# Kernel tuning notes

Measured on AMD Instinct MI355X. Metric: run time of the kernel, lower is better.

## Reference

```python
import jax, jax.numpy as jnp
import numpy as np


def setup_inputs() -> dict:
    key = jax.random.key(0)
    inputs = jax.random.normal(key, (4096, 8192), dtype=jnp.float32)
    return {"inputs": inputs, "k": 512}


def reference(inputs, k):
    # Original: kth_smallest = sort_ascending(inputs)[..., n-1-k]
    # i.e. the (k+1)-th largest value per row. Equivalent via top_k.
    # Keep only elements STRICTLY greater than that threshold.
    thresh = jax.lax.top_k(inputs, k + 1)[0][..., -1]  # [batch]
    mask = (inputs > thresh[:, None]).astype(inputs.dtype)
    return inputs * mask
```

## Files before the change

kernel.cpp:

```cpp
#include <hip/hip_runtime.h>
#include <stdint.h>


constexpr int COLS  = 8192;
constexpr int TPB   = 256;
constexpr int EPT   = COLS / TPB;
constexpr int VPT   = EPT / 4;
constexpr int NBIN0 = 2048;
constexpr int CAP   = 2048;

typedef float f32x4 __attribute__((ext_vector_type(4)));

__device__ __forceinline__ uint32_t map_f32(uint32_t u) {
  return (u & 0x80000000u) ? ~u : (u | 0x80000000u);
}
__device__ __forceinline__ float unmap_f32(uint32_t m) {
  return __uint_as_float((m & 0x80000000u) ? (m ^ 0x80000000u) : ~m);
}

template <int RPB>
__global__ __launch_bounds__(TPB, 4)
void ksparse_kernel(const float* __restrict__ in, const int* __restrict__ kptr,
                    float* __restrict__ out) {
  __shared__ __align__(16) uint32_t hist[2 * NBIN0];
  __shared__ uint32_t th[3 * 128];
  __shared__ uint32_t wtot[4];
  __shared__ uint32_t s_packed;
  __shared__ uint32_t s_cnt;
  __shared__ uint32_t s_sel[3];

  const int t    = threadIdx.x;
  const int wave = t >> 6;
  const int lane = t & 63;
  const size_t row0 = (size_t)blockIdx.x * RPB;

  const uint32_t kbase = (uint32_t)(*kptr) + 1u;

  float4   v[2][VPT];
  uint32_t m[EPT];

  {
    const float4* inp = (const float4*)(in + row0 * COLS);
#pragma unroll
    for (int i = 0; i < VPT; ++i) v[0][i] = inp[t + i * TPB];
  }

#pragma unroll
  for (int r = 0; r < RPB; ++r) {
    uint4* h4 = (uint4*)hist;
#pragma unroll
    for (int i = 0; i < 4; ++i) h4[t + i * TPB] = make_uint4(0u, 0u, 0u, 0u);
    th[t] = 0u;
    if (t < 128) th[256 + t] = 0u;
    if (t == 0) { s_packed = 0u; s_cnt = 0u; }
    uint32_t kk = kbase;
    __syncthreads();

    uint32_t* h = &hist[(wave >> 1) * NBIN0];
#pragma unroll
    for (int i = 0; i < VPT; ++i) {
      m[4 * i + 0] = map_f32(__float_as_uint(v[r & 1][i].x));
      m[4 * i + 1] = map_f32(__float_as_uint(v[r & 1][i].y));
      m[4 * i + 2] = map_f32(__float_as_uint(v[r & 1][i].z));
      m[4 * i + 3] = map_f32(__float_as_uint(v[r & 1][i].w));
      atomicAdd(&h[m[4 * i + 0] >> 21], 1u);
      atomicAdd(&h[m[4 * i + 1] >> 21], 1u);
      atomicAdd(&h[m[4 * i + 2] >> 21], 1u);
      atomicAdd(&h[m[4 * i + 3] >> 21], 1u);
    }

    if (r + 1 < RPB) {
      const float4* inp = (const float4*)(in + (row0 + (size_t)(r + 1)) * COLS);
#pragma unroll
      for (int i = 0; i < VPT; ++i) v[(r + 1) & 1][i] = inp[t + i * TPB];
    }
    __syncthreads();

    {
      const uint4* hv = (const uint4*)hist;
      uint4 a0 = hv[2 * t], a1 = hv[2 * t + 1];
      uint4 b0 = hv[512 + 2 * t], b1 = hv[512 + 2 * t + 1];
      uint32_t c0 = a0.x + b0.x, c1 = a0.y + b0.y, c2 = a0.z + b0.z, c3 = a0.w + b0.w;
      uint32_t c4 = a1.x + b1.x, c5 = a1.y + b1.y, c6 = a1.z + b1.z, c7 = a1.w + b1.w;
      uint32_t sl[8];
      sl[7] = c7;         sl[6] = sl[7] + c6; sl[5] = sl[6] + c5; sl[4] = sl[5] + c4;
      sl[3] = sl[4] + c3; sl[2] = sl[3] + c2; sl[1] = sl[2] + c1; sl[0] = sl[1] + c0;
      const uint32_t total = sl[0];

      uint32_t s = total;
#pragma unroll
      for (int off = 1; off < 64; off <<= 1) {
        uint32_t tmp = __shfl_down(s, off, 64);
        s += (lane + off < 64) ? tmp : 0u;
      }
      if (lane == 0) wtot[wave] = s;
      __syncthreads();

      uint32_t hi = 0;
#pragma unroll
      for (int w = 1; w < 4; ++w)
        if (w > wave) hi += wtot[w];
      const uint32_t excl = hi + (s - total);

      int best = -1;
#pragma unroll
      for (int j = 7; j >= 0; --j)
        if (best < 0 && excl + sl[j] >= kk) best = j;
      if (best >= 0) {
        const uint32_t above = excl + ((best < 7) ? sl[best + 1] : 0u);
        atomicMax(&s_packed, ((uint32_t)(t * 8 + best) << 14) | above);
      }
    }
    __syncthreads();

    const uint32_t pk = s_packed;
    const uint32_t d0 = pk >> 14;
    kk -= (pk & 0x3FFFu);

    uint32_t* cand = &hist[NBIN0];
#pragma unroll
    for (int i = 0; i < EPT; ++i) {
      if ((m[i] >> 21) == d0) {
        uint32_t idx = atomicAdd(&s_cnt, 1u);
        if (idx < CAP) cand[idx] = m[i] & 0x1FFFFFu;
      }
    }
    __syncthreads();
    const uint32_t Cc = (s_cnt < (uint32_t)CAP) ? s_cnt : (uint32_t)CAP;

    uint32_t tpref = 0;
#pragma unroll 1
    for (int j = 0; j < 3; ++j) {
      const int dsh = 14 - 7 * j;
      uint32_t* thj = &th[j * 128];
      for (uint32_t idx = t; idx < Cc; idx += TPB) {
        const uint32_t c = cand[idx];
        const bool ok = (j == 0) || ((c >> (dsh + 7)) == tpref);
        if (ok) atomicAdd(&thj[(c >> dsh) & 127u], 1u);
      }
      __syncthreads();

      if (wave == 0) {
        uint32_t a = thj[lane], b = thj[64 + lane];
        uint32_t sb = b, sa = a;
#pragma unroll
        for (int off = 1; off < 64; off <<= 1) {
          uint32_t t1 = __shfl_down(sb, off, 64);
          uint32_t t2 = __shfl_down(sa, off, 64);
          const bool inr = (lane + off < 64);
          sb += inr ? t1 : 0u;
          sa += inr ? t2 : 0u;
        }
        const uint32_t tb = __shfl(sb, 0, 64);
        sa += tb;
        const unsigned long long mb = __ballot(sb >= kk);
        uint32_t d, ab;
        if (mb) {
          const int hb = 63 - __builtin_clzll(mb);
          const uint32_t nx = __shfl(sb, (hb + 1) & 63, 64);
          d = 64 + hb;
          ab = (hb == 63) ? 0u : nx;
        } else {
          const unsigned long long ma = __ballot(sa >= kk);
          const int ha = 63 - __builtin_clzll(ma);
          const uint32_t nx = __shfl(sa, (ha + 1) & 63, 64);
          d = (uint32_t)ha;
          ab = (ha == 63) ? tb : nx;
        }
        if (lane == 0) s_sel[j] = (d << 16) | ab;
      }
      __syncthreads();

      const uint32_t sel = s_sel[j];
      tpref = (tpref << 7) | (sel >> 16);
      kk -= (sel & 0xFFFFu);
    }

    const uint32_t T = (d0 << 21) | tpref;

    f32x4* op = (f32x4*)(out + (row0 + (size_t)r) * COLS);
#pragma unroll
    for (int i = 0; i < VPT; ++i) {
      f32x4 w;
      uint32_t mm;
      mm = m[4 * i + 0]; w.x = (mm > T) ? unmap_f32(mm) : 0.0f;
      mm = m[4 * i + 1]; w.y = (mm > T) ? unmap_f32(mm) : 0.0f;
      mm = m[4 * i + 2]; w.z = (mm > T) ? unmap_f32(mm) : 0.0f;
      mm = m[4 * i + 3]; w.w = (mm > T) ? unmap_f32(mm) : 0.0f;
      __builtin_nontemporal_store(w, &op[t + i * TPB]);
    }
  }
}

extern "C" void kernel_launch(void* const* d_in, const int* in_sizes, int n_in,
                              void* d_out, int out_size, void* d_ws, size_t ws_size,
                              hipStream_t stream) {
  const float* in  = (const float*)d_in[0];
  const int*   k   = (const int*)d_in[1];
  float*       out = (float*)d_out;
  int rows = in_sizes[0] / COLS;
  if (rows < 1) rows = 1;
  if ((rows & 3) == 0) {
    ksparse_kernel<4><<<rows / 4, TPB, 0, stream>>>(in, k, out);
  } else {
    ksparse_kernel<1><<<rows, TPB, 0, stream>>>(in, k, out);
  }
}
```

Baseline: 258.7 us.

## Process rows of a block concurrently in lockstep instead of sequentially

Each block now handles two rows at once. Both rows are loaded up front and each gets its own histogram, and every selection phase runs for both rows between shared barriers, which halves the number of barrier-separated phases per row. The refinement scans run on separate waves per row. The per-wave split histogram is dropped, so histogram atomics contend on a single copy per row. Nontemporal output stores become plain stores. This holds more registers per thread (two rows of values and mapped keys) and doubles the block count, which can hurt occupancy.

```diff
diff --git a/kernel.cpp b/kernel.cpp
--- a/kernel.cpp
+++ b/kernel.cpp
@@ -9,8 +9,6 @@
 constexpr int NBIN0 = 2048;
 constexpr int CAP   = 2048;
 
-typedef float f32x4 __attribute__((ext_vector_type(4)));
-
 __device__ __forceinline__ uint32_t map_f32(uint32_t u) {
   return (u & 0x80000000u) ? ~u : (u | 0x80000000u);
 }
@@ -22,172 +20,204 @@
 __global__ __launch_bounds__(TPB, 4)
 void ksparse_kernel(const float* __restrict__ in, const int* __restrict__ kptr,
                     float* __restrict__ out) {
-  __shared__ __align__(16) uint32_t hist[2 * NBIN0];
-  __shared__ uint32_t th[3 * 128];
-  __shared__ uint32_t wtot[4];
-  __shared__ uint32_t s_packed;
-  __shared__ uint32_t s_cnt;
-  __shared__ uint32_t s_sel[3];
+  constexpr int NH = (RPB > 1) ? RPB : 2;
+  __shared__ __align__(16) uint32_t hist[NH * NBIN0];
+  __shared__ uint32_t th[RPB * 3 * 128];
+  __shared__ uint32_t wtot[RPB][4];
+  __shared__ uint32_t s_packed[RPB];
+  __shared__ uint32_t s_cnt[RPB];
+  __shared__ uint32_t s_sel[RPB][3];
 
   const int t    = threadIdx.x;
   const int wave = t >> 6;
   const int lane = t & 63;
-  const size_t row0 = (size_t)blockIdx.x * RPB;
-
+  const size_t rowbase = (size_t)blockIdx.x * RPB * COLS;
+
+  const float4* inp = (const float4*)(in + rowbase);
+  float4 v[RPB][VPT];
+#pragma unroll
+  for (int r = 0; r < RPB; ++r)
+#pragma unroll
+    for (int i = 0; i < VPT; ++i)
+      v[r][i] = inp[r * (COLS / 4) + t + i * TPB];
+
+  uint4* h4 = (uint4*)hist;
+#pragma unroll
+  for (int i = 0; i < NH * NBIN0 / 4 / TPB; ++i)
+    h4[t + i * TPB] = make_uint4(0u, 0u, 0u, 0u);
+#pragma unroll
+  for (int i = 0; i < (RPB * 384 + TPB - 1) / TPB; ++i) {
+    const int idx = t + i * TPB;
+    if (idx < RPB * 384) th[idx] = 0u;
+  }
+  if (t < RPB) { s_packed[t] = 0u; s_cnt[t] = 0u; }
   const uint32_t kbase = (uint32_t)(*kptr) + 1u;
-
-  float4   v[2][VPT];
-  uint32_t m[EPT];
-
-  {
-    const float4* inp = (const float4*)(in + row0 * COLS);
-#pragma unroll
-    for (int i = 0; i < VPT; ++i) v[0][i] = inp[t + i * TPB];
-  }
-
-#pragma unroll
-  for (int r = 0; r < RPB; ++r) {
-    uint4* h4 = (uint4*)hist;
-#pragma unroll
-    for (int i = 0; i < 4; ++i) h4[t + i * TPB] = make_uint4(0u, 0u, 0u, 0u);
-    th[t] = 0u;
-    if (t < 128) th[256 + t] = 0u;
-    if (t == 0) { s_packed = 0u; s_cnt = 0u; }
-    uint32_t kk = kbase;
+  __syncthreads();
+
+  uint32_t m[RPB][EPT];
+#pragma unroll
+  for (int r = 0; r < RPB; ++r) {
+    uint32_t* h = &hist[r * NBIN0];
+#pragma unroll
+    for (int i = 0; i < VPT; ++i) {
+      m[r][4 * i + 0] = map_f32(__float_as_uint(v[r][i].x));
+      m[r][4 * i + 1] = map_f32(__float_as_uint(v[r][i].y));
+      m[r][4 * i + 2] = map_f32(__float_as_uint(v[r][i].z));
+      m[r][4 * i + 3] = map_f32(__float_as_uint(v[r][i].w));
+      atomicAdd(&h[m[r][4 * i + 0] >> 21], 1u);
+      atomicAdd(&h[m[r][4 * i + 1] >> 21], 1u);
+      atomicAdd(&h[m[r][4 * i + 2] >> 21], 1u);
+      atomicAdd(&h[m[r][4 * i + 3] >> 21], 1u);
+    }
+  }
+  __syncthreads();
+
+  uint32_t kk[RPB];
+  uint32_t sl0[RPB];
+  uint32_t ssum[RPB];
+  uint4    sva0[RPB], sva1[RPB];
+#pragma unroll
+  for (int r = 0; r < RPB; ++r) {
+    kk[r] = kbase;
+    const uint4* hv = (const uint4*)&hist[r * NBIN0];
+    const uint4 a0 = hv[2 * t], a1 = hv[2 * t + 1];
+    sva0[r] = a0; sva1[r] = a1;
+    const uint32_t total = a0.x + a0.y + a0.z + a0.w + a1.x + a1.y + a1.z + a1.w;
+    sl0[r] = total;
+
+    uint32_t s = total;
+#pragma unroll
+    for (int off = 1; off < 64; off <<= 1) {
+      const uint32_t tmp = __shfl_down(s, off, 64);
+      s += (lane + off < 64) ? tmp : 0u;
+    }
+    ssum[r] = s;
+    if (lane == 0) wtot[r][wave] = s;
+  }
+  __syncthreads();
+
+#pragma unroll
+  for (int r = 0; r < RPB; ++r) {
+    uint32_t hi = 0;
+#pragma unroll
+    for (int w = 1; w < 4; ++w)
+      if (w > wave) hi += wtot[r][w];
+    const uint32_t excl = hi + (ssum[r] - sl0[r]);
+
+    const uint4 a0 = sva0[r], a1 = sva1[r];
+    uint32_t sl[8];
+    sl[7] = a1.w;         sl[6] = sl[7] + a1.z; sl[5] = sl[6] + a1.y; sl[4] = sl[5] + a1.x;
+    sl[3] = sl[4] + a0.w; sl[2] = sl[3] + a0.z; sl[1] = sl[2] + a0.y; sl[0] = sl[1] + a0.x;
+
+    int b = -1;
+#pragma unroll
+    for (int j = 7; j >= 0; --j)
+      if (b < 0 && excl + sl[j] >= kk[r]) b = j;
+    if (b >= 0) {
+      const uint32_t above = excl + ((b < 7) ? sl[b + 1] : 0u);
+      atomicMax(&s_packed[r], ((uint32_t)(t * 8 + b) << 14) | above);
+    }
+  }
+  __syncthreads();
+
+  uint32_t d0[RPB];
+#pragma unroll
+  for (int r = 0; r < RPB; ++r) {
+    const uint32_t pk = s_packed[r];
+    d0[r] = pk >> 14;
+    kk[r] -= (pk & 0x3FFFu);
+    uint32_t* cand = &hist[(RPB == 1 ? 1 : r) * NBIN0];
+#pragma unroll
+    for (int i = 0; i < EPT; ++i) {
+      if ((m[r][i] >> 21) == d0[r]) {
+        const uint32_t idx = atomicAdd(&s_cnt[r], 1u);
+        if (idx < CAP) cand[idx] = m[r][i] & 0x1FFFFFu;
+      }
+    }
+  }
+  __syncthreads();
+  uint32_t Cc[RPB];
+#pragma unroll
+  for (int r = 0; r < RPB; ++r)
+    Cc[r] = (s_cnt[r] < (uint32_t)CAP) ? s_cnt[r] : (uint32_t)CAP;
+
+  uint32_t tpref[RPB];
+#pragma unroll
+  for (int r = 0; r < RPB; ++r) tpref[r] = 0;
+
+#pragma unroll 1
+  for (int j = 0; j < 3; ++j) {
+    const int dsh = 14 - 7 * j;
+#pragma unroll
+    for (int r = 0; r < RPB; ++r) {
+      uint32_t* thj = &th[(r * 3 + j) * 128];
+      uint32_t* cand = &hist[(RPB == 1 ? 1 : r) * NBIN0];
+      for (uint32_t idx = t; idx < Cc[r]; idx += TPB) {
+        const uint32_t c = cand[idx];
+        const bool ok = (j == 0) || ((c >> (dsh + 7)) == tpref[r]);
+        if (ok) atomicAdd(&thj[(c >> dsh) & 127u], 1u);
+      }
+    }
     __syncthreads();
 
-    uint32_t* h = &hist[(wave >> 1) * NBIN0];
+    if (wave < RPB) {
+      uint32_t kw = 0;
+      uint32_t* thj = &th[j * 128];
+#pragma unroll
+      for (int r = 0; r < RPB; ++r)
+        if (wave == r) { kw = kk[r]; thj = &th[(r * 3 + j) * 128]; }
+
+      const uint32_t a = thj[lane], b = thj[64 + lane];
+      uint32_t sb = b, sa = a;
+#pragma unroll
+      for (int off = 1; off < 64; off <<= 1) {
+        const uint32_t t1 = __shfl_down(sb, off, 64);
+        const uint32_t t2 = __shfl_down(sa, off, 64);
+        const bool inr = (lane + off < 64);
+        sb += inr ? t1 : 0u;
+        sa += inr ? t2 : 0u;
+      }
+      const uint32_t tb = __shfl(sb, 0, 64);
+      sa += tb;
+      const unsigned long long mb = __ballot(sb >= kw);
+      uint32_t d, ab;
+      if (mb) {
+        const int hb = 63 - __builtin_clzll(mb);
+        const uint32_t nx = __shfl(sb, (hb + 1) & 63, 64);
+        d = 64 + (uint32_t)hb;
+        ab = (hb == 63) ? 0u : nx;
+      } else {
+        const unsigned long long ma = __ballot(sa >= kw);
+        const int ha = 63 - __builtin_clzll(ma);
+        const uint32_t nx = __shfl(sa, (ha + 1) & 63, 64);
+        d = (uint32_t)ha;
+        ab = (ha == 63) ? tb : nx;
+      }
+      if (lane == 0) s_sel[wave][j] = (d << 16) | ab;
+    }
+    __syncthreads();
+
+#pragma unroll
+    for (int r = 0; r < RPB; ++r) {
+      const uint32_t sel = s_sel[r][j];
+      tpref[r] = (tpref[r] << 7) | (sel >> 16);
+      kk[r] -= (sel & 0xFFFFu);
+    }
+  }
+
+  float4* op = (float4*)(out + rowbase);
+#pragma unroll
+  for (int r = 0; r < RPB; ++r) {
+    const uint32_t T = (d0[r] << 21) | tpref[r];
 #pragma unroll
     for (int i = 0; i < VPT; ++i) {
-      m[4 * i + 0] = map_f32(__float_as_uint(v[r & 1][i].x));
-      m[4 * i + 1] = map_f32(__float_as_uint(v[r & 1][i].y));
-      m[4 * i + 2] = map_f32(__float_as_uint(v[r & 1][i].z));
-      m[4 * i + 3] = map_f32(__float_as_uint(v[r & 1][i].w));
-      atomicAdd(&h[m[4 * i + 0] >> 21], 1u);
-      atomicAdd(&h[m[4 * i + 1] >> 21], 1u);
-      atomicAdd(&h[m[4 * i + 2] >> 21], 1u);
-      atomicAdd(&h[m[4 * i + 3] >> 21], 1u);
-    }
-
-    if (r + 1 < RPB) {
-      const float4* inp = (const float4*)(in + (row0 + (size_t)(r + 1)) * COLS);
-#pragma unroll
-      for (int i = 0; i < VPT; ++i) v[(r + 1) & 1][i] = inp[t + i * TPB];
-    }
-    __syncthreads();
-
-    {
-      const uint4* hv = (const uint4*)hist;
-      uint4 a0 = hv[2 * t], a1 = hv[2 * t + 1];
-      uint4 b0 = hv[512 + 2 * t], b1 = hv[512 + 2 * t + 1];
-      uint32_t c0 = a0.x + b0.x, c1 = a0.y + b0.y, c2 = a0.z + b0.z, c3 = a0.w + b0.w;
-      uint32_t c4 = a1.x + b1.x, c5 = a1.y + b1.y, c6 = a1.z + b1.z, c7 = a1.w + b1.w;
-      uint32_t sl[8];
-      sl[7] = c7;         sl[6] = sl[7] + c6; sl[5] = sl[6] + c5; sl[4] = sl[5] + c4;
-      sl[3] = sl[4] + c3; sl[2] = sl[3] + c2; sl[1] = sl[2] + c1; sl[0] = sl[1] + c0;
-      const uint32_t total = sl[0];
-
-      uint32_t s = total;
-#pragma unroll
-      for (int off = 1; off < 64; off <<= 1) {
-        uint32_t tmp = __shfl_down(s, off, 64);
-        s += (lane + off < 64) ? tmp : 0u;
-      }
-      if (lane == 0) wtot[wave] = s;
-      __syncthreads();
-
-      uint32_t hi = 0;
-#pragma unroll
-      for (int w = 1; w < 4; ++w)
-        if (w > wave) hi += wtot[w];
-      const uint32_t excl = hi + (s - total);
-
-      int best = -1;
-#pragma unroll
-      for (int j = 7; j >= 0; --j)
-        if (best < 0 && excl + sl[j] >= kk) best = j;
-      if (best >= 0) {
-        const uint32_t above = excl + ((best < 7) ? sl[best + 1] : 0u);
-        atomicMax(&s_packed, ((uint32_t)(t * 8 + best) << 14) | above);
-      }
-    }
-    __syncthreads();
-
-    const uint32_t pk = s_packed;
-    const uint32_t d0 = pk >> 14;
-    kk -= (pk & 0x3FFFu);
-
-    uint32_t* cand = &hist[NBIN0];
-#pragma unroll
-    for (int i = 0; i < EPT; ++i) {
-      if ((m[i] >> 21) == d0) {
-        uint32_t idx = atomicAdd(&s_cnt, 1u);
-        if (idx < CAP) cand[idx] = m[i] & 0x1FFFFFu;
-      }
-    }
-    __syncthreads();
-    const uint32_t Cc = (s_cnt < (uint32_t)CAP) ? s_cnt : (uint32_t)CAP;
-
-    uint32_t tpref = 0;
-#pragma unroll 1
-    for (int j = 0; j < 3; ++j) {
-      const int dsh = 14 - 7 * j;
-      uint32_t* thj = &th[j * 128];
-      for (uint32_t idx = t; idx < Cc; idx += TPB) {
-        const uint32_t c = cand[idx];
-        const bool ok = (j == 0) || ((c >> (dsh + 7)) == tpref);
-        if (ok) atomicAdd(&thj[(c >> dsh) & 127u], 1u);
-      }
-      __syncthreads();
-
-      if (wave == 0) {
-        uint32_t a = thj[lane], b = thj[64 + lane];
-        uint32_t sb = b, sa = a;
-#pragma unroll
-        for (int off = 1; off < 64; off <<= 1) {
-          uint32_t t1 = __shfl_down(sb, off, 64);
-          uint32_t t2 = __shfl_down(sa, off, 64);
-          const bool inr = (lane + off < 64);
-          sb += inr ? t1 : 0u;
-          sa += inr ? t2 : 0u;
-        }
-        const uint32_t tb = __shfl(sb, 0, 64);
-        sa += tb;
-        const unsigned long long mb = __ballot(sb >= kk);
-        uint32_t d, ab;
-        if (mb) {
-          const int hb = 63 - __builtin_clzll(mb);
-          const uint32_t nx = __shfl(sb, (hb + 1) & 63, 64);
-          d = 64 + hb;
-          ab = (hb == 63) ? 0u : nx;
-        } else {
-          const unsigned long long ma = __ballot(sa >= kk);
-          const int ha = 63 - __builtin_clzll(ma);
-          const uint32_t nx = __shfl(sa, (ha + 1) & 63, 64);
-          d = (uint32_t)ha;
-          ab = (ha == 63) ? tb : nx;
-        }
-        if (lane == 0) s_sel[j] = (d << 16) | ab;
-      }
-      __syncthreads();
-
-      const uint32_t sel = s_sel[j];
-      tpref = (tpref << 7) | (sel >> 16);
-      kk -= (sel & 0xFFFFu);
-    }
-
-    const uint32_t T = (d0 << 21) | tpref;
-
-    f32x4* op = (f32x4*)(out + (row0 + (size_t)r) * COLS);
-#pragma unroll
-    for (int i = 0; i < VPT; ++i) {
-      f32x4 w;
+      float4 w;
       uint32_t mm;
-      mm = m[4 * i + 0]; w.x = (mm > T) ? unmap_f32(mm) : 0.0f;
-      mm = m[4 * i + 1]; w.y = (mm > T) ? unmap_f32(mm) : 0.0f;
-      mm = m[4 * i + 2]; w.z = (mm > T) ? unmap_f32(mm) : 0.0f;
-      mm = m[4 * i + 3]; w.w = (mm > T) ? unmap_f32(mm) : 0.0f;
-      __builtin_nontemporal_store(w, &op[t + i * TPB]);
+      mm = m[r][4 * i + 0]; w.x = (mm > T) ? unmap_f32(mm) : 0.0f;
+      mm = m[r][4 * i + 1]; w.y = (mm > T) ? unmap_f32(mm) : 0.0f;
+      mm = m[r][4 * i + 2]; w.z = (mm > T) ? unmap_f32(mm) : 0.0f;
+      mm = m[r][4 * i + 3]; w.w = (mm > T) ? unmap_f32(mm) : 0.0f;
+      op[r * (COLS / 4) + t + i * TPB] = w;
     }
   }
 }
@@ -200,8 +230,8 @@
   float*       out = (float*)d_out;
   int rows = in_sizes[0] / COLS;
   if (rows < 1) rows = 1;
-  if ((rows & 3) == 0) {
-    ksparse_kernel<4><<<rows / 4, TPB, 0, stream>>>(in, k, out);
+  if ((rows & 1) == 0) {
+    ksparse_kernel<2><<<rows / 2, TPB, 0, stream>>>(in, k, out);
   } else {
     ksparse_kernel<1><<<rows, TPB, 0, stream>>>(in, k, out);
   }
```

New measurement: 247.0 us. 1.05x faster.
